# Kernel optimization log

Measured on AMD Instinct MI355X. Metric: run time of the kernel, lower is better.

Reference implementation:

```python
import jax, jax.numpy as jnp
import numpy as np

H = 16
N_JOBS = 1000000
N_MACH = 500000
NEG = -1e8

PARAM_SHAPES = [("jW1",(H,H)),("jb1",(H,)),("jW2",(H,H)),("jb2",(H,)),
                ("mW1",(H,H)),("mb1",(H,)),("mW2",(H,H)),("mb2",(H,)),
                ("aj_Wq",(H,H)),("aj_bq",(H,)),("aj_Wr",(H,H)),("aj_V",(H,)),
                ("am_Wq",(H,H)),("am_bq",(H,)),("am_Wr",(H,H)),("am_V",(H,)),
                ("ja_Wq",(H,H)),("ja_bq",(H,)),("ja_Wr",(H,H)),("ja_V",(H,)),
                ("ma_Wq",(H,H)),("ma_bq",(H,)),("ma_Wr",(H,H)),("ma_V",(H,)),
                ("g1W",(H,3*H)),("g1b",(H,)),("g2W",(H,3*H)),("g2b",(H,)),
                ("last_j",(H,))]

def setup_inputs() -> dict:
    key = jax.random.key(0)
    inp = {}
    inp["jobs"] = jax.random.normal(jax.random.fold_in(key, 0), (N_JOBS, H), dtype=jnp.float32)
    inp["machines"] = jax.random.normal(jax.random.fold_in(key, 1), (N_MACH, H), dtype=jnp.float32)
    inp["alloc_jobs_mask"] = jax.random.randint(jax.random.fold_in(key, 2), (N_JOBS,), 0, 2) > 0
    for i, (name, shape) in enumerate(PARAM_SHAPES):
        inp[name] = jax.random.normal(jax.random.fold_in(key, 10 + i), shape, dtype=jnp.float32) * 0.05
    return inp

def _emb(x, W1, b1, W2, b2):
    # custom_embedding: two tanh MLP layers (torch Linear: x @ W.T + b)
    h = jnp.tanh(x @ W1.T + b1)
    return jnp.tanh(h @ W2.T + b2)

def _att_logits(q, ref, Wq, bq, Wr, V):
    # Bahdanau additive attention: tanh(W_q q + W_r ref) @ V -> [S]
    return jnp.tanh((q @ Wq.T + bq) + ref @ Wr.T) @ V

def _query_att(q, ref, Wq, bq, Wr, V):
    # Attention with use_softmax=True followed by weighted sum over ref
    w = jax.nn.softmax(_att_logits(q, ref, Wq, bq, Wr, V))
    return w @ ref  # [H]

def reference(jobs, machines, alloc_jobs_mask,
              jW1, jb1, jW2, jb2, mW1, mb1, mW2, mb2,
              aj_Wq, aj_bq, aj_Wr, aj_V, am_Wq, am_bq, am_Wr, am_V,
              ja_Wq, ja_bq, ja_Wr, ja_V, ma_Wq, ma_bq, ma_Wr, ma_V,
              g1W, g1b, g2W, g2b, last_j):
    E_j = _emb(jobs, jW1, jb1, jW2, jb2)        # [Sj, H]
    E_m = _emb(machines, mW1, mb1, mW2, mb2)    # [Sm, H]

    # glimpse 1 conditioned on last_j
    g_j1 = _query_att(last_j, E_j, aj_Wq, aj_bq, aj_Wr, aj_V)
    g_m1 = _query_att(last_j, E_m, am_Wq, am_bq, am_Wr, am_V)
    g1 = jnp.tanh(jnp.concatenate([last_j, g_j1, g_m1]) @ g1W.T + g1b)

    # job pointer logits + invalid-action masking
    j_logits = _att_logits(g1, E_j, ja_Wq, ja_bq, ja_Wr, ja_V)
    j_logits = jnp.where(alloc_jobs_mask, j_logits, NEG)
    sel_j = jnp.argmax(j_logits)
    e_js = E_j[sel_j]

    # glimpse 2 conditioned on selected job embedding
    g_j2 = _query_att(e_js, E_j, aj_Wq, aj_bq, aj_Wr, aj_V)
    g_m2 = _query_att(e_js, E_m, am_Wq, am_bq, am_Wr, am_V)
    g2 = jnp.tanh(jnp.concatenate([e_js, g_j2, g_m2]) @ g2W.T + g2b)

    m_logits = _att_logits(g2, E_m, ma_Wq, ma_bq, ma_Wr, ma_V)
    sel_m = jnp.argmax(m_logits)

    logpas = jax.nn.log_softmax(j_logits)[sel_j] + jax.nn.log_softmax(m_logits)[sel_m]
    return sel_j, sel_m, logpas
```

## Files before the change

kernel.cpp:

```cpp
#include <hip/hip_runtime.h>
#include <cstddef>
#include <cstdint>


constexpr int NJ = 1000000;
constexpr int NM = 500000;
constexpr float NEGV = -1e8f;

constexpr int BLK = 256;
constexpr int ROWS_PER_BLK = 512;
constexpr int GB_J2 = (NJ + ROWS_PER_BLK - 1) / ROWS_PER_BLK;
constexpr int GB_M2 = (NM + ROWS_PER_BLK - 1) / ROWS_PER_BLK;
constexpr int GB_TOT2 = GB_J2 + GB_M2;

constexpr int S_QKJA = 0;
constexpr int S_QK2J = 16;
constexpr int S_QK2M = 32;
constexpr int S_EJS  = 48;
constexpr int S_QKMA = 64;
constexpr int S_LOGPJ = 80;
constexpr int S_SELJ  = 81;
constexpr int S_QK1J  = 96;
constexpr int S_QK1M  = 112;
constexpr int P1J = 128;
constexpr int P1M = P1J + GB_J2 * 17;
constexpr int P2V = P1M + GB_M2 * 17;
constexpr int P2I = P2V + GB_J2;
constexpr int P2L = P2I + GB_J2;
constexpr size_t E_OFF = 65536;
static_assert(P2L + GB_J2 <= (int)E_OFF, "partials overflow into E cache");

typedef float v2f __attribute__((ext_vector_type(2)));

struct Params {
    const float *jobs, *machines;
    const int *mask;
    const float *jW1, *jb1, *jW2, *jb2;
    const float *mW1, *mb1, *mW2, *mb2;
    const float *aj_Wq, *aj_bq, *aj_Wr, *aj_V;
    const float *am_Wq, *am_bq, *am_Wr, *am_V;
    const float *ja_Wq, *ja_bq, *ja_Wr, *ja_V;
    const float *ma_Wq, *ma_bq, *ma_Wr, *ma_V;
    const float *g1W, *g1b, *g2W, *g2b, *last_j;
    float *S;
    float *Ej, *Em;
    float *out;
};


__device__ __forceinline__ float fast_tanh(float x) {
    float e = __expf(2.0f * x);
    return 1.0f - __fdividef(2.0f, e + 1.0f);
}

__device__ __forceinline__ v2f vbc(float a) { v2f r; r.x = a; r.y = a; return r; }

__device__ __forceinline__ v2f vfma(float w, v2f b, v2f c) {
    return __builtin_elementwise_fma(vbc(w), b, c);
}
__device__ __forceinline__ v2f vfma2(v2f a, v2f b, v2f c) {
    return __builtin_elementwise_fma(a, b, c);
}
__device__ __forceinline__ v2f vtanh(v2f a) {
    v2f r; r.x = fast_tanh(a.x); r.y = fast_tanh(a.y); return r;
}

__device__ __forceinline__ void load16(const float* __restrict__ X, size_t r, float (&x)[16]) {
    const float4* p4 = reinterpret_cast<const float4*>(X) + r * 4;
    float4 a = p4[0], b = p4[1], c = p4[2], d = p4[3];
    x[0]=a.x; x[1]=a.y; x[2]=a.z; x[3]=a.w;
    x[4]=b.x; x[5]=b.y; x[6]=b.z; x[7]=b.w;
    x[8]=c.x; x[9]=c.y; x[10]=c.z; x[11]=c.w;
    x[12]=d.x; x[13]=d.y; x[14]=d.z; x[15]=d.w;
}

__device__ __forceinline__ void load16_v2(const float* __restrict__ X, size_t rA, size_t rB,
                                          v2f (&x)[16]) {
    float a[16], b[16];
    load16(X, rA, a);
    load16(X, rB, b);
#pragma unroll
    for (int k = 0; k < 16; ++k) { x[k].x = a[k]; x[k].y = b[k]; }
}

__device__ __forceinline__ void store16_lane(float* __restrict__ X, size_t r,
                                             const v2f (&x)[16], int lane) {
    float4* p4 = reinterpret_cast<float4*>(X) + r * 4;
    if (lane == 0) {
        p4[0] = make_float4(x[0].x, x[1].x, x[2].x, x[3].x);
        p4[1] = make_float4(x[4].x, x[5].x, x[6].x, x[7].x);
        p4[2] = make_float4(x[8].x, x[9].x, x[10].x, x[11].x);
        p4[3] = make_float4(x[12].x, x[13].x, x[14].x, x[15].x);
    } else {
        p4[0] = make_float4(x[0].y, x[1].y, x[2].y, x[3].y);
        p4[1] = make_float4(x[4].y, x[5].y, x[6].y, x[7].y);
        p4[2] = make_float4(x[8].y, x[9].y, x[10].y, x[11].y);
        p4[3] = make_float4(x[12].y, x[13].y, x[14].y, x[15].y);
    }
}

__device__ __forceinline__ void emb16_v2(const v2f (&x)[16],
                                         const float* __restrict__ W1, const float* __restrict__ b1,
                                         const float* __restrict__ W2, const float* __restrict__ b2,
                                         v2f (&e)[16]) {
    v2f h[16];
#pragma unroll
    for (int i = 0; i < 16; ++i) {
        v2f a = vbc(b1[i]);
#pragma unroll
        for (int k = 0; k < 16; ++k) a = vfma(W1[i * 16 + k], x[k], a);
        h[i] = vtanh(a);
    }
#pragma unroll
    for (int i = 0; i < 16; ++i) {
        v2f a = vbc(b2[i]);
#pragma unroll
        for (int k = 0; k < 16; ++k) a = vfma(W2[i * 16 + k], h[k], a);
        e[i] = vtanh(a);
    }
}

__device__ __forceinline__ v2f att_logit_v2(const v2f (&e)[16], const float (&qk)[16],
                                            const float* __restrict__ Wr,
                                            const float* __restrict__ V) {
    v2f acc = vbc(0.0f);
#pragma unroll
    for (int i = 0; i < 16; ++i) {
        v2f r = vbc(qk[i]);
#pragma unroll
        for (int k = 0; k < 16; ++k) r = vfma(Wr[i * 16 + k], e[k], r);
        acc = vfma2(vbc(V[i]), vtanh(r), acc);
    }
    return acc;
}

__device__ __forceinline__ float wave_reduce_sum(float v) {
#pragma unroll
    for (int off = 32; off > 0; off >>= 1) v += __shfl_xor(v, off, 64);
    return v;
}

__device__ __forceinline__ void wave_reduce_argmax(float &v, int &idx) {
#pragma unroll
    for (int off = 32; off > 0; off >>= 1) {
        float ov = __shfl_xor(v, off, 64);
        int oi = __shfl_xor(idx, off, 64);
        if (ov > v || (ov == v && oi < idx)) { v = ov; idx = oi; }
    }
}

__device__ __forceinline__ float block_sum(float v) {
    __shared__ float sm[4];
    v = wave_reduce_sum(v);
    __syncthreads();
    if ((threadIdx.x & 63) == 0) sm[threadIdx.x >> 6] = v;
    __syncthreads();
    return sm[0] + sm[1] + sm[2] + sm[3];
}

__device__ __forceinline__ void block_argmax(float &v, int &i) {
    __shared__ float sv[4];
    __shared__ int si[4];
    wave_reduce_argmax(v, i);
    __syncthreads();
    if ((threadIdx.x & 63) == 0) { sv[threadIdx.x >> 6] = v; si[threadIdx.x >> 6] = i; }
    __syncthreads();
    float bv = sv[0]; int bi = si[0];
#pragma unroll
    for (int k = 1; k < 4; ++k)
        if (sv[k] > bv || (sv[k] == bv && si[k] < bi)) { bv = sv[k]; bi = si[k]; }
    v = bv; i = bi;
}

__device__ __forceinline__ void block_sum17(float l, float (&s)[16], float* dst) {
    l = wave_reduce_sum(l);
#pragma unroll
    for (int i = 0; i < 16; ++i) s[i] = wave_reduce_sum(s[i]);
    __shared__ float red[4][17];
    int w = threadIdx.x >> 6, ln = threadIdx.x & 63;
    if (ln == 0) {
        red[w][0] = l;
#pragma unroll
        for (int i = 0; i < 16; ++i) red[w][1 + i] = s[i];
    }
    __syncthreads();
    if (threadIdx.x < 17)
        dst[threadIdx.x] = red[0][threadIdx.x] + red[1][threadIdx.x] + red[2][threadIdx.x] + red[3][threadIdx.x];
}

__global__ __launch_bounds__(64) void k_init(Params p) {
    if (threadIdx.x < 32) {
        const bool isJ = threadIdx.x < 16;
        const int i = threadIdx.x & 15;
        const float* Wq = isJ ? p.aj_Wq : p.am_Wq;
        const float* bq = isJ ? p.aj_bq : p.am_bq;
        float a = bq[i];
#pragma unroll
        for (int k = 0; k < 16; ++k) a = fmaf(Wq[i * 16 + k], p.last_j[k], a);
        p.S[(isJ ? S_QK1J : S_QK1M) + i] = a;
    }
}

template <bool CACHE>
__global__ __launch_bounds__(BLK) void k_emb_g1(Params p) {
    const bool isJob = blockIdx.x < GB_J2;
    const float* X  = isJob ? p.jobs : p.machines;
    const float* W1 = isJob ? p.jW1 : p.mW1;
    const float* b1 = isJob ? p.jb1 : p.mb1;
    const float* W2 = isJob ? p.jW2 : p.mW2;
    const float* b2 = isJob ? p.jb2 : p.mb2;
    const float* Wr = isJob ? p.aj_Wr : p.am_Wr;
    const float* V  = isJob ? p.aj_V  : p.am_V;
    float* E = isJob ? p.Ej : p.Em;
    const int n  = isJob ? NJ : NM;
    const int b0 = isJob ? (int)blockIdx.x : (int)blockIdx.x - GB_J2;

    float qk[16];
    {
        const float* src = p.S + (isJob ? S_QK1J : S_QK1M);
#pragma unroll
        for (int i = 0; i < 16; ++i) qk[i] = src[i];
    }

    const int r0 = b0 * ROWS_PER_BLK + (int)threadIdx.x;
    const int r1 = r0 + BLK;
    const bool v0 = r0 < n, v1 = r1 < n;
    const size_t a0 = (size_t)(v0 ? r0 : 0);
    const size_t a1 = (size_t)(v1 ? r1 : 0);

    v2f x[16], e[16];
    load16_v2(X, a0, a1, x);
    emb16_v2(x, W1, b1, W2, b2, e);
    if (CACHE) {
        if (v0) store16_lane(E, a0, e, 0);
        if (v1) store16_lane(E, a1, e, 1);
    }
    v2f lg = att_logit_v2(e, qk, Wr, V);
    float pw0 = v0 ? __expf(lg.x) : 0.0f;
    float pw1 = v1 ? __expf(lg.y) : 0.0f;
    float l = pw0 + pw1, s[16];
#pragma unroll
    for (int i = 0; i < 16; ++i) s[i] = fmaf(pw0, e[i].x, pw1 * e[i].y);

    block_sum17(l, s, p.S + (isJob ? P1J : P1M) + (size_t)b0 * 17);
}

__global__ __launch_bounds__(BLK) void k_combine_g(Params p, int phase) {
    const float* PJ = p.S + P1J;
    const float* PM = p.S + P1M;
    float accJ[17], accM[17];
#pragma unroll
    for (int c = 0; c < 17; ++c) { accJ[c] = 0.0f; accM[c] = 0.0f; }
    for (int i = threadIdx.x; i < GB_J2; i += BLK)
#pragma unroll
        for (int c = 0; c < 17; ++c) accJ[c] += PJ[i * 17 + c];
    for (int i = threadIdx.x; i < GB_M2; i += BLK)
#pragma unroll
        for (int c = 0; c < 17; ++c) accM[c] += PM[i * 17 + c];

    __shared__ float totJ[17], totM[17];
    for (int c = 0; c < 17; ++c) {
        float t = block_sum(accJ[c]);
        if (threadIdx.x == 0) totJ[c] = t;
        t = block_sum(accM[c]);
        if (threadIdx.x == 0) totM[c] = t;
    }
    __syncthreads();

    __shared__ float cb[48], gbuf[16];
    if (threadIdx.x < 16) {
        int i = threadIdx.x;
        cb[i]      = phase ? p.S[S_EJS + i] : p.last_j[i];
        cb[16 + i] = totJ[1 + i] / totJ[0];
        cb[32 + i] = totM[1 + i] / totM[0];
    }
    __syncthreads();
    const float* gW  = phase ? p.g2W : p.g1W;
    const float* gbv = phase ? p.g2b : p.g1b;
    if (threadIdx.x < 16) {
        int i = threadIdx.x;
        float a = gbv[i];
#pragma unroll
        for (int k = 0; k < 48; ++k) a = fmaf(gW[i * 48 + k], cb[k], a);
        gbuf[i] = fast_tanh(a);
    }
    __syncthreads();
    const float* Wq = phase ? p.ma_Wq : p.ja_Wq;
    const float* bq = phase ? p.ma_bq : p.ja_bq;
    const int off = phase ? S_QKMA : S_QKJA;
    if (threadIdx.x < 16) {
        int i = threadIdx.x;
        float a = bq[i];
#pragma unroll
        for (int k = 0; k < 16; ++k) a = fmaf(Wq[i * 16 + k], gbuf[k], a);
        p.S[off + i] = a;
    }
}

template <bool CACHE>
__global__ __launch_bounds__(BLK) void k_jlogits(Params p) {
    float qk[16];
#pragma unroll
    for (int i = 0; i < 16; ++i) qk[i] = p.S[S_QKJA + i];

    const int r0 = blockIdx.x * ROWS_PER_BLK + (int)threadIdx.x;
    const int r1 = r0 + BLK;
    const bool v0 = r0 < NJ, v1 = r1 < NJ;
    const size_t a0 = (size_t)(v0 ? r0 : 0);
    const size_t a1 = (size_t)(v1 ? r1 : 0);

    v2f e[16];
    if (CACHE) {
        load16_v2(p.Ej, a0, a1, e);
    } else {
        v2f x[16];
        load16_v2(p.jobs, a0, a1, x);
        emb16_v2(x, p.jW1, p.jb1, p.jW2, p.jb2, e);
    }
    v2f lg = att_logit_v2(e, qk, p.ja_Wr, p.ja_V);
    const bool m0 = v0 && (p.mask[a0] != 0);
    const bool m1 = v1 && (p.mask[a1] != 0);
    float l = (m0 ? __expf(lg.x) : 0.0f) + (m1 ? __expf(lg.y) : 0.0f);
    float am0 = m0 ? lg.x : NEGV - 1.0f;
    float am1 = m1 ? lg.y : NEGV - 1.0f;
    float best;
    int bi;
    if (am0 >= am1) { best = am0; bi = r0; }
    else            { best = am1; bi = r1; }

    l = wave_reduce_sum(l);
    wave_reduce_argmax(best, bi);
    __shared__ float rl[4], rv[4];
    __shared__ int ri[4];
    int w = threadIdx.x >> 6, ln = threadIdx.x & 63;
    if (ln == 0) { rl[w] = l; rv[w] = best; ri[w] = bi; }
    __syncthreads();
    if (threadIdx.x == 0) {
        float L = rl[0] + rl[1] + rl[2] + rl[3];
        float v = rv[0]; int i = ri[0];
#pragma unroll
        for (int k = 1; k < 4; ++k)
            if (rv[k] > v || (rv[k] == v && ri[k] < i)) { v = rv[k]; i = ri[k]; }
        p.S[P2V + blockIdx.x] = v;
        p.S[P2I + blockIdx.x] = (float)i;
        p.S[P2L + blockIdx.x] = L;
    }
}

__global__ __launch_bounds__(BLK) void k_combine2(Params p) {
    float v = -3.4e38f; int vi = 0x7fffffff; float l = 0.0f;
    for (int i = threadIdx.x; i < GB_J2; i += BLK) {
        float pv = p.S[P2V + i];
        int pi = (int)p.S[P2I + i];
        if (pv > v || (pv == v && pi < vi)) { v = pv; vi = pi; }
        l += p.S[P2L + i];
    }
    l = block_sum(l);
    block_argmax(v, vi);
    const int sel = vi;

    __shared__ float xb[16], hb[16], eb[16];
    if (threadIdx.x < 16) xb[threadIdx.x] = p.jobs[(size_t)sel * 16 + threadIdx.x];
    __syncthreads();
    if (threadIdx.x < 16) {
        int i = threadIdx.x;
        float a = p.jb1[i];
#pragma unroll
        for (int k = 0; k < 16; ++k) a = fmaf(p.jW1[i * 16 + k], xb[k], a);
        hb[i] = fast_tanh(a);
    }
    __syncthreads();
    if (threadIdx.x < 16) {
        int i = threadIdx.x;
        float a = p.jb2[i];
#pragma unroll
        for (int k = 0; k < 16; ++k) a = fmaf(p.jW2[i * 16 + k], hb[k], a);
        float e = fast_tanh(a);
        eb[i] = e;
        p.S[S_EJS + i] = e;
    }
    __syncthreads();
    if (threadIdx.x < 16) {
        int i = threadIdx.x;
        float a1 = p.aj_bq[i], a2 = p.am_bq[i];
#pragma unroll
        for (int k = 0; k < 16; ++k) {
            a1 = fmaf(p.aj_Wq[i * 16 + k], eb[k], a1);
            a2 = fmaf(p.am_Wq[i * 16 + k], eb[k], a2);
        }
        p.S[S_QK2J + i] = a1;
        p.S[S_QK2M + i] = a2;
    }
    if (threadIdx.x == 0) {
        p.S[S_LOGPJ] = v - logf(l);
        p.S[S_SELJ] = (float)sel;
    }
}

template <bool CACHE>
__global__ __launch_bounds__(BLK) void k_glimpse2(Params p) {
    const bool isJob = blockIdx.x < GB_J2;
    const float* Wr = isJob ? p.aj_Wr : p.am_Wr;
    const float* V  = isJob ? p.aj_V  : p.am_V;
    const float* E  = isJob ? p.Ej : p.Em;
    const float* X  = isJob ? p.jobs : p.machines;
    const float* W1 = isJob ? p.jW1 : p.mW1;
    const float* b1 = isJob ? p.jb1 : p.mb1;
    const float* W2 = isJob ? p.jW2 : p.mW2;
    const float* b2 = isJob ? p.jb2 : p.mb2;
    const int n  = isJob ? NJ : NM;
    const int b0 = isJob ? (int)blockIdx.x : (int)blockIdx.x - GB_J2;
    const int qoff = isJob ? S_QK2J : S_QK2M;

    float qk[16];
#pragma unroll
    for (int i = 0; i < 16; ++i) qk[i] = p.S[qoff + i];

    const int r0 = b0 * ROWS_PER_BLK + (int)threadIdx.x;
    const int r1 = r0 + BLK;
    const bool v0 = r0 < n, v1 = r1 < n;
    const size_t a0 = (size_t)(v0 ? r0 : 0);
    const size_t a1 = (size_t)(v1 ? r1 : 0);

    v2f e[16];
    if (CACHE) {
        load16_v2(E, a0, a1, e);
    } else {
        v2f x[16];
        load16_v2(X, a0, a1, x);
        emb16_v2(x, W1, b1, W2, b2, e);
    }
    v2f lg = att_logit_v2(e, qk, Wr, V);
    float pw0 = v0 ? __expf(lg.x) : 0.0f;
    float pw1 = v1 ? __expf(lg.y) : 0.0f;
    float l = pw0 + pw1, s[16];
#pragma unroll
    for (int i = 0; i < 16; ++i) s[i] = fmaf(pw0, e[i].x, pw1 * e[i].y);

    block_sum17(l, s, p.S + (isJob ? P1J : P1M) + (size_t)b0 * 17);
}

template <bool CACHE>
__global__ __launch_bounds__(BLK) void k_mlogits(Params p) {
    float qk[16];
#pragma unroll
    for (int i = 0; i < 16; ++i) qk[i] = p.S[S_QKMA + i];

    const int r0 = blockIdx.x * ROWS_PER_BLK + (int)threadIdx.x;
    const int r1 = r0 + BLK;
    const bool v0 = r0 < NM, v1 = r1 < NM;
    const size_t a0 = (size_t)(v0 ? r0 : 0);
    const size_t a1 = (size_t)(v1 ? r1 : 0);

    v2f e[16];
    if (CACHE) {
        load16_v2(p.Em, a0, a1, e);
    } else {
        v2f x[16];
        load16_v2(p.machines, a0, a1, x);
        emb16_v2(x, p.mW1, p.mb1, p.mW2, p.mb2, e);
    }
    v2f lg = att_logit_v2(e, qk, p.ma_Wr, p.ma_V);
    float l = (v0 ? __expf(lg.x) : 0.0f) + (v1 ? __expf(lg.y) : 0.0f);
    float am0 = v0 ? lg.x : -3.4e38f;
    float am1 = v1 ? lg.y : -3.4e38f;
    float best;
    int bi;
    if (am0 >= am1) { best = am0; bi = r0; }
    else            { best = am1; bi = r1; }

    l = wave_reduce_sum(l);
    wave_reduce_argmax(best, bi);
    __shared__ float rl[4], rv[4];
    __shared__ int ri[4];
    int w = threadIdx.x >> 6, ln = threadIdx.x & 63;
    if (ln == 0) { rl[w] = l; rv[w] = best; ri[w] = bi; }
    __syncthreads();
    if (threadIdx.x == 0) {
        float L = rl[0] + rl[1] + rl[2] + rl[3];
        float v = rv[0]; int i = ri[0];
#pragma unroll
        for (int k = 1; k < 4; ++k)
            if (rv[k] > v || (rv[k] == v && ri[k] < i)) { v = rv[k]; i = ri[k]; }
        p.S[P2V + blockIdx.x] = v;
        p.S[P2I + blockIdx.x] = (float)i;
        p.S[P2L + blockIdx.x] = L;
    }
}

__global__ __launch_bounds__(BLK) void k_combine4(Params p) {
    float v = -3.4e38f; int vi = 0x7fffffff; float l = 0.0f;
    for (int i = threadIdx.x; i < GB_M2; i += BLK) {
        float pv = p.S[P2V + i];
        int pi = (int)p.S[P2I + i];
        if (pv > v || (pv == v && pi < vi)) { v = pv; vi = pi; }
        l += p.S[P2L + i];
    }
    l = block_sum(l);
    block_argmax(v, vi);
    if (threadIdx.x == 0) {
        p.out[0] = p.S[S_SELJ];
        p.out[1] = (float)vi;
        p.out[2] = p.S[S_LOGPJ] + (v - logf(l));
    }
}

extern "C" void kernel_launch(void* const* d_in, const int* in_sizes, int n_in,
                              void* d_out, int out_size, void* d_ws, size_t ws_size,
                              hipStream_t stream) {
    Params p;
    p.jobs     = (const float*)d_in[0];
    p.machines = (const float*)d_in[1];
    p.mask     = (const int*)d_in[2];
    p.jW1 = (const float*)d_in[3];  p.jb1 = (const float*)d_in[4];
    p.jW2 = (const float*)d_in[5];  p.jb2 = (const float*)d_in[6];
    p.mW1 = (const float*)d_in[7];  p.mb1 = (const float*)d_in[8];
    p.mW2 = (const float*)d_in[9];  p.mb2 = (const float*)d_in[10];
    p.aj_Wq = (const float*)d_in[11]; p.aj_bq = (const float*)d_in[12];
    p.aj_Wr = (const float*)d_in[13]; p.aj_V  = (const float*)d_in[14];
    p.am_Wq = (const float*)d_in[15]; p.am_bq = (const float*)d_in[16];
    p.am_Wr = (const float*)d_in[17]; p.am_V  = (const float*)d_in[18];
    p.ja_Wq = (const float*)d_in[19]; p.ja_bq = (const float*)d_in[20];
    p.ja_Wr = (const float*)d_in[21]; p.ja_V  = (const float*)d_in[22];
    p.ma_Wq = (const float*)d_in[23]; p.ma_bq = (const float*)d_in[24];
    p.ma_Wr = (const float*)d_in[25]; p.ma_V  = (const float*)d_in[26];
    p.g1W = (const float*)d_in[27]; p.g1b = (const float*)d_in[28];
    p.g2W = (const float*)d_in[29]; p.g2b = (const float*)d_in[30];
    p.last_j = (const float*)d_in[31];
    p.S = (float*)d_ws;
    p.Ej = (float*)d_ws + E_OFF;
    p.Em = p.Ej + (size_t)NJ * 16;
    p.out = (float*)d_out;

    const size_t needed = (E_OFF + (size_t)(NJ + NM) * 16) * sizeof(float);
    const bool cache = ws_size >= needed;

    k_init<<<1, 64, 0, stream>>>(p);
    if (cache) {
        k_emb_g1<true><<<GB_TOT2, BLK, 0, stream>>>(p);
        k_combine_g<<<1, BLK, 0, stream>>>(p, 0);
        k_jlogits<true><<<GB_J2, BLK, 0, stream>>>(p);
        k_combine2<<<1, BLK, 0, stream>>>(p);
        k_glimpse2<true><<<GB_TOT2, BLK, 0, stream>>>(p);
        k_combine_g<<<1, BLK, 0, stream>>>(p, 1);
        k_mlogits<true><<<GB_M2, BLK, 0, stream>>>(p);
        k_combine4<<<1, BLK, 0, stream>>>(p);
    } else {
        k_emb_g1<false><<<GB_TOT2, BLK, 0, stream>>>(p);
        k_combine_g<<<1, BLK, 0, stream>>>(p, 0);
        k_jlogits<false><<<GB_J2, BLK, 0, stream>>>(p);
        k_combine2<<<1, BLK, 0, stream>>>(p);
        k_glimpse2<false><<<GB_TOT2, BLK, 0, stream>>>(p);
        k_combine_g<<<1, BLK, 0, stream>>>(p, 1);
        k_mlogits<false><<<GB_M2, BLK, 0, stream>>>(p);
        k_combine4<<<1, BLK, 0, stream>>>(p);
    }
}
```

Before: 337.5 us.

## Use block-tiled embedding cache layout, fuse query init, cheaper tanh

The embedding cache is stored in a block-interleaved layout. Each thread now owns two adjacent rows, and the pair is written and read as eight float4 values strided by the thread count, so cache traffic is fully coalesced. The separate init kernel is removed: each block recomputes the first-glimpse query projection into shared memory. tanh now uses the hardware exp2 and rcp intrinsics, and combine_g uses the batched block_sum17 in place of 34 serial block reductions. The cached E layout becomes private to this kernel, and the input row loads are now pairs of adjacent rows rather than rows one block-width apart.

```diff
diff --git a/kernel.cpp b/kernel.cpp
--- a/kernel.cpp
+++ b/kernel.cpp
@@ -12,6 +12,7 @@
 constexpr int GB_J2 = (NJ + ROWS_PER_BLK - 1) / ROWS_PER_BLK;
 constexpr int GB_M2 = (NM + ROWS_PER_BLK - 1) / ROWS_PER_BLK;
 constexpr int GB_TOT2 = GB_J2 + GB_M2;
+constexpr int EBLK = ROWS_PER_BLK * 16;
 
 constexpr int S_QKJA = 0;
 constexpr int S_QK2J = 16;
@@ -20,8 +21,6 @@
 constexpr int S_QKMA = 64;
 constexpr int S_LOGPJ = 80;
 constexpr int S_SELJ  = 81;
-constexpr int S_QK1J  = 96;
-constexpr int S_QK1M  = 112;
 constexpr int P1J = 128;
 constexpr int P1M = P1J + GB_J2 * 17;
 constexpr int P2V = P1M + GB_M2 * 17;
@@ -49,8 +48,9 @@
 
 
 __device__ __forceinline__ float fast_tanh(float x) {
-    float e = __expf(2.0f * x);
-    return 1.0f - __fdividef(2.0f, e + 1.0f);
+    float e = __builtin_amdgcn_exp2f(x * 2.8853900817779268f);
+    float r = __builtin_amdgcn_rcpf(e + 1.0f);
+    return fmaf(-2.0f, r, 1.0f);
 }
 
 __device__ __forceinline__ v2f vbc(float a) { v2f r; r.x = a; r.y = a; return r; }
@@ -83,19 +83,19 @@
     for (int k = 0; k < 16; ++k) { x[k].x = a[k]; x[k].y = b[k]; }
 }
 
-__device__ __forceinline__ void store16_lane(float* __restrict__ X, size_t r,
-                                             const v2f (&x)[16], int lane) {
-    float4* p4 = reinterpret_cast<float4*>(X) + r * 4;
-    if (lane == 0) {
-        p4[0] = make_float4(x[0].x, x[1].x, x[2].x, x[3].x);
-        p4[1] = make_float4(x[4].x, x[5].x, x[6].x, x[7].x);
-        p4[2] = make_float4(x[8].x, x[9].x, x[10].x, x[11].x);
-        p4[3] = make_float4(x[12].x, x[13].x, x[14].x, x[15].x);
-    } else {
-        p4[0] = make_float4(x[0].y, x[1].y, x[2].y, x[3].y);
-        p4[1] = make_float4(x[4].y, x[5].y, x[6].y, x[7].y);
-        p4[2] = make_float4(x[8].y, x[9].y, x[10].y, x[11].y);
-        p4[3] = make_float4(x[12].y, x[13].y, x[14].y, x[15].y);
+__device__ __forceinline__ void ecache_store(float* __restrict__ Eb, int t, const v2f (&e)[16]) {
+    float4* p4 = reinterpret_cast<float4*>(Eb);
+#pragma unroll
+    for (int kp = 0; kp < 8; ++kp)
+        p4[kp * 256 + t] = make_float4(e[2*kp].x, e[2*kp].y, e[2*kp+1].x, e[2*kp+1].y);
+}
+__device__ __forceinline__ void ecache_load(const float* __restrict__ Eb, int t, v2f (&e)[16]) {
+    const float4* p4 = reinterpret_cast<const float4*>(Eb);
+#pragma unroll
+    for (int kp = 0; kp < 8; ++kp) {
+        float4 q = p4[kp * 256 + t];
+        e[2*kp].x = q.x;   e[2*kp].y = q.y;
+        e[2*kp+1].x = q.z; e[2*kp+1].y = q.w;
     }
 }
 
@@ -178,6 +178,7 @@
     for (int i = 0; i < 16; ++i) s[i] = wave_reduce_sum(s[i]);
     __shared__ float red[4][17];
     int w = threadIdx.x >> 6, ln = threadIdx.x & 63;
+    __syncthreads();
     if (ln == 0) {
         red[w][0] = l;
 #pragma unroll
@@ -186,19 +187,6 @@
     __syncthreads();
     if (threadIdx.x < 17)
         dst[threadIdx.x] = red[0][threadIdx.x] + red[1][threadIdx.x] + red[2][threadIdx.x] + red[3][threadIdx.x];
-}
-
-__global__ __launch_bounds__(64) void k_init(Params p) {
-    if (threadIdx.x < 32) {
-        const bool isJ = threadIdx.x < 16;
-        const int i = threadIdx.x & 15;
-        const float* Wq = isJ ? p.aj_Wq : p.am_Wq;
-        const float* bq = isJ ? p.aj_bq : p.am_bq;
-        float a = bq[i];
-#pragma unroll
-        for (int k = 0; k < 16; ++k) a = fmaf(Wq[i * 16 + k], p.last_j[k], a);
-        p.S[(isJ ? S_QK1J : S_QK1M) + i] = a;
-    }
 }
 
 template <bool CACHE>
@@ -215,15 +203,23 @@
     const int n  = isJob ? NJ : NM;
     const int b0 = isJob ? (int)blockIdx.x : (int)blockIdx.x - GB_J2;
 
+    __shared__ float qks[16];
+    if (threadIdx.x < 16) {
+        const float* Wq = isJob ? p.aj_Wq : p.am_Wq;
+        const float* bq = isJob ? p.aj_bq : p.am_bq;
+        const int i = threadIdx.x;
+        float a = bq[i];
+#pragma unroll
+        for (int k = 0; k < 16; ++k) a = fmaf(Wq[i * 16 + k], p.last_j[k], a);
+        qks[i] = a;
+    }
+    __syncthreads();
     float qk[16];
-    {
-        const float* src = p.S + (isJob ? S_QK1J : S_QK1M);
-#pragma unroll
-        for (int i = 0; i < 16; ++i) qk[i] = src[i];
-    }
-
-    const int r0 = b0 * ROWS_PER_BLK + (int)threadIdx.x;
-    const int r1 = r0 + BLK;
+#pragma unroll
+    for (int i = 0; i < 16; ++i) qk[i] = qks[i];
+
+    const int r0 = b0 * ROWS_PER_BLK + 2 * (int)threadIdx.x;
+    const int r1 = r0 + 1;
     const bool v0 = r0 < n, v1 = r1 < n;
     const size_t a0 = (size_t)(v0 ? r0 : 0);
     const size_t a1 = (size_t)(v1 ? r1 : 0);
@@ -231,10 +227,7 @@
     v2f x[16], e[16];
     load16_v2(X, a0, a1, x);
     emb16_v2(x, W1, b1, W2, b2, e);
-    if (CACHE) {
-        if (v0) store16_lane(E, a0, e, 0);
-        if (v1) store16_lane(E, a1, e, 1);
-    }
+    if (CACHE) ecache_store(E + (size_t)b0 * EBLK, (int)threadIdx.x, e);
     v2f lg = att_logit_v2(e, qk, Wr, V);
     float pw0 = v0 ? __expf(lg.x) : 0.0f;
     float pw1 = v1 ? __expf(lg.y) : 0.0f;
@@ -248,23 +241,22 @@
 __global__ __launch_bounds__(BLK) void k_combine_g(Params p, int phase) {
     const float* PJ = p.S + P1J;
     const float* PM = p.S + P1M;
-    float accJ[17], accM[17];
-#pragma unroll
-    for (int c = 0; c < 17; ++c) { accJ[c] = 0.0f; accM[c] = 0.0f; }
-    for (int i = threadIdx.x; i < GB_J2; i += BLK)
-#pragma unroll
-        for (int c = 0; c < 17; ++c) accJ[c] += PJ[i * 17 + c];
-    for (int i = threadIdx.x; i < GB_M2; i += BLK)
-#pragma unroll
-        for (int c = 0; c < 17; ++c) accM[c] += PM[i * 17 + c];
-
+    float lJ = 0.0f, lM = 0.0f, sJ[16], sM[16];
+#pragma unroll
+    for (int c = 0; c < 16; ++c) { sJ[c] = 0.0f; sM[c] = 0.0f; }
+    for (int i = threadIdx.x; i < GB_J2; i += BLK) {
+        lJ += PJ[i * 17];
+#pragma unroll
+        for (int c = 0; c < 16; ++c) sJ[c] += PJ[i * 17 + 1 + c];
+    }
+    for (int i = threadIdx.x; i < GB_M2; i += BLK) {
+        lM += PM[i * 17];
+#pragma unroll
+        for (int c = 0; c < 16; ++c) sM[c] += PM[i * 17 + 1 + c];
+    }
     __shared__ float totJ[17], totM[17];
-    for (int c = 0; c < 17; ++c) {
-        float t = block_sum(accJ[c]);
-        if (threadIdx.x == 0) totJ[c] = t;
-        t = block_sum(accM[c]);
-        if (threadIdx.x == 0) totM[c] = t;
-    }
+    block_sum17(lJ, sJ, totJ);
+    block_sum17(lM, sM, totM);
     __syncthreads();
 
     __shared__ float cb[48], gbuf[16];
@@ -303,15 +295,15 @@
 #pragma unroll
     for (int i = 0; i < 16; ++i) qk[i] = p.S[S_QKJA + i];
 
-    const int r0 = blockIdx.x * ROWS_PER_BLK + (int)threadIdx.x;
-    const int r1 = r0 + BLK;
+    const int r0 = blockIdx.x * ROWS_PER_BLK + 2 * (int)threadIdx.x;
+    const int r1 = r0 + 1;
     const bool v0 = r0 < NJ, v1 = r1 < NJ;
     const size_t a0 = (size_t)(v0 ? r0 : 0);
     const size_t a1 = (size_t)(v1 ? r1 : 0);
 
     v2f e[16];
     if (CACHE) {
-        load16_v2(p.Ej, a0, a1, e);
+        ecache_load(p.Ej + (size_t)blockIdx.x * EBLK, (int)threadIdx.x, e);
     } else {
         v2f x[16];
         load16_v2(p.jobs, a0, a1, x);
@@ -416,15 +408,15 @@
 #pragma unroll
     for (int i = 0; i < 16; ++i) qk[i] = p.S[qoff + i];
 
-    const int r0 = b0 * ROWS_PER_BLK + (int)threadIdx.x;
-    const int r1 = r0 + BLK;
+    const int r0 = b0 * ROWS_PER_BLK + 2 * (int)threadIdx.x;
+    const int r1 = r0 + 1;
     const bool v0 = r0 < n, v1 = r1 < n;
     const size_t a0 = (size_t)(v0 ? r0 : 0);
     const size_t a1 = (size_t)(v1 ? r1 : 0);
 
     v2f e[16];
     if (CACHE) {
-        load16_v2(E, a0, a1, e);
+        ecache_load(E + (size_t)b0 * EBLK, (int)threadIdx.x, e);
     } else {
         v2f x[16];
         load16_v2(X, a0, a1, x);
@@ -446,15 +438,15 @@
 #pragma unroll
     for (int i = 0; i < 16; ++i) qk[i] = p.S[S_QKMA + i];
 
-    const int r0 = blockIdx.x * ROWS_PER_BLK + (int)threadIdx.x;
-    const int r1 = r0 + BLK;
+    const int r0 = blockIdx.x * ROWS_PER_BLK + 2 * (int)threadIdx.x;
+    const int r1 = r0 + 1;
     const bool v0 = r0 < NM, v1 = r1 < NM;
     const size_t a0 = (size_t)(v0 ? r0 : 0);
     const size_t a1 = (size_t)(v1 ? r1 : 0);
 
     v2f e[16];
     if (CACHE) {
-        load16_v2(p.Em, a0, a1, e);
+        ecache_load(p.Em + (size_t)blockIdx.x * EBLK, (int)threadIdx.x, e);
     } else {
         v2f x[16];
         load16_v2(p.machines, a0, a1, x);
@@ -529,13 +521,12 @@
     p.last_j = (const float*)d_in[31];
     p.S = (float*)d_ws;
     p.Ej = (float*)d_ws + E_OFF;
-    p.Em = p.Ej + (size_t)NJ * 16;
+    p.Em = p.Ej + (size_t)GB_J2 * EBLK;
     p.out = (float*)d_out;
 
-    const size_t needed = (E_OFF + (size_t)(NJ + NM) * 16) * sizeof(float);
+    const size_t needed = (E_OFF + (size_t)GB_TOT2 * EBLK) * sizeof(float);
     const bool cache = ws_size >= needed;
 
-    k_init<<<1, 64, 0, stream>>>(p);
     if (cache) {
         k_emb_g1<true><<<GB_TOT2, BLK, 0, stream>>>(p);
         k_combine_g<<<1, BLK, 0, stream>>>(p, 0);
```

New measurement: 304.7 us. -9.7%, faster.
